# Performance work log

Measured on AMD Instinct MI355X. Metric: run time of the kernel, lower is better.

## Reference

```python
import jax, jax.numpy as jnp
import numpy as np

B, C, N, H, W = 8, 128, 16, 56, 56
HID, OUT = 128, 128


def conv1x1(x, w, b):
    # 1x1x1 Conv3d == channel-mixing GEMM. x: [B,Cin,N,H,W], w: [Cout,Cin], b: [Cout]
    return jnp.einsum('oc,bcnhw->bonhw', w, x) + b[None, :, None, None, None]


def setup_inputs() -> dict:
    key = jax.random.key(0)
    ks = jax.random.split(key, 9)
    s = 0.02
    return {
        'x': jax.random.normal(ks[0], (B, C, N, H, W), dtype=jnp.float32),
        'w_q': jax.random.normal(ks[1], (HID, C), dtype=jnp.float32) * s,
        'b_q': jax.random.normal(ks[2], (HID,), dtype=jnp.float32) * s,
        'w_k': jax.random.normal(ks[3], (HID, C), dtype=jnp.float32) * s,
        'b_k': jax.random.normal(ks[4], (HID,), dtype=jnp.float32) * s,
        'w_v': jax.random.normal(ks[5], (HID, C), dtype=jnp.float32) * s,
        'b_v': jax.random.normal(ks[6], (HID,), dtype=jnp.float32) * s,
        'w_o': jax.random.normal(ks[7], (OUT, HID), dtype=jnp.float32) * s,
        'b_o': jax.random.normal(ks[8], (OUT,), dtype=jnp.float32) * s,
    }


def reference(x, w_q, b_q, w_k, b_k, w_v, b_v, w_o, b_o):
    Bsz, Cc, Nn, Hh, Ww = x.shape
    L = Nn * Hh * Ww
    q = conv1x1(x, w_q, b_q).reshape(Bsz, -1, L)   # [B, hid, L]
    k = conv1x1(x, w_k, b_k).reshape(Bsz, -1, L)   # [B, hid, L]
    v = conv1x1(x, w_v, b_v).reshape(Bsz, -1, L)   # [B, hid, L]
    # NOTE: attention is over CHANNELS (hid x hid), since k was transposed to [B, L, hid]
    attn = jax.nn.softmax(jnp.einsum('bql,bkl->bqk', q, k), axis=-1)  # [B, hid, hid]
    feats = jnp.einsum('bqk,bkl->bql', attn, v).reshape(Bsz, -1, Nn, Hh, Ww)
    out = conv1x1(feats, w_o, b_o) + x             # residual requires out_dim == in_dim
    return jnp.mean(out, axis=2)                   # mean over N (depth) -> [B, out, H, W]
```

## Files before the change

kernel.cpp:

```cpp
#include <hip/hip_runtime.h>
#include <hip/hip_bf16.h>
#include <cstdint>

#define BB   8
#define CCH  128
#define NND  16
#define HWD  3136
#define LLT  50176
#define HWB  64
#define NHB  49

#define OFF_SP  0
#define OFF_RP  6422528
#define OFF_S   6472704
#define OFF_M   6603776
#define OFF_Q   6734848
#define OFF_AV  6865920
#define OFF_CV  6866944

typedef __attribute__((ext_vector_type(8)))  short bf16x8;
typedef __attribute__((ext_vector_type(16))) float f32x16;

__device__ __forceinline__ uint32_t fbits(float f){ union{float f;uint32_t u;}v; v.f=f; return v.u; }
__device__ __forceinline__ float bitsf(uint32_t u){ union{uint32_t u;float f;}v; v.u=u; return v.f; }

#define MFMA32(a,b,c) __builtin_amdgcn_mfma_f32_32x32x16_bf16((a),(b),(c),0,0,0)

__global__ __launch_bounds__(256,2) void k1_gram(const float* __restrict__ x,
    float* __restrict__ Sp, float* __restrict__ rp, float* __restrict__ Y)
{
  __shared__ __align__(16) short lds_h[2][8*128*8];
  __shared__ __align__(16) short lds_l[2][8*128*8];
  const int b   = blockIdx.x / NHB;
  const int hb  = blockIdx.x % NHB;
  const int hw0 = hb * HWB;
  const int tid = threadIdx.x;
  const int lane = tid & 63, w = tid >> 6;
  const int wr = w >> 1, wc = w & 1;
  const int rr  = tid >> 1, h = tid & 1;
  const float* xb = x + (size_t)b*CCH*LLT + (size_t)rr*LLT + hw0 + 32*h;

  f32x16 acc[2][2];
  #pragma unroll
  for(int ai=0;ai<2;ai++)
    #pragma unroll
    for(int bi=0;bi<2;bi++)
      #pragma unroll
      for(int e=0;e<16;e++) acc[ai][bi][e] = 0.f;
  float yac[32];
  #pragma unroll
  for(int i=0;i<32;i++) yac[i]=0.f;

  float4 v[8];
  #pragma unroll
  for(int u=0;u<8;u++) v[u] = *(const float4*)(xb + 4*u);

#define SPLIT(bufi)                                                         \
  {                                                                         \
    _Pragma("unroll")                                                       \
    for(int c2=0;c2<4;c2++){                                                \
      int hwd_[4], lwd_[4];                                                 \
      _Pragma("unroll")                                                     \
      for(int q=0;q<2;q++){                                                 \
        const int u = 2*c2+q;                                               \
        const float x0=v[u].x, x1=v[u].y, x2=v[u].z, x3=v[u].w;             \
        const uint32_t a0=fbits(x0),a1=fbits(x1),a2=fbits(x2),a3=fbits(x3); \
        hwd_[2*q+0] = __builtin_amdgcn_perm(a1, a0, 0x07060302u);           \
        hwd_[2*q+1] = __builtin_amdgcn_perm(a3, a2, 0x07060302u);           \
        const float l0 = x0 - bitsf(a0&0xFFFF0000u);                        \
        const float l1 = x1 - bitsf(a1&0xFFFF0000u);                        \
        const float l2 = x2 - bitsf(a2&0xFFFF0000u);                        \
        const float l3 = x3 - bitsf(a3&0xFFFF0000u);                        \
        lwd_[2*q+0] = __builtin_amdgcn_perm(fbits(l1), fbits(l0), 0x07060302u); \
        lwd_[2*q+1] = __builtin_amdgcn_perm(fbits(l3), fbits(l2), 0x07060302u); \
        yac[4*u+0]+=x0; yac[4*u+1]+=x1; yac[4*u+2]+=x2; yac[4*u+3]+=x3;     \
      }                                                                     \
      const int kc = 4*h + c2;                                              \
      *(int4*)&lds_h[bufi][(kc*128 + rr)*8] = make_int4(hwd_[0],hwd_[1],hwd_[2],hwd_[3]); \
      *(int4*)&lds_l[bufi][(kc*128 + rr)*8] = make_int4(lwd_[0],lwd_[1],lwd_[2],lwd_[3]); \
    }                                                                       \
  }

  SPLIT(0);
  __syncthreads();
  #pragma unroll
  for(int u=0;u<8;u++) v[u] = *(const float4*)(xb + HWD + 4*u);

  for(int n=0;n<NND;n++){
    const int cur = n & 1;
    #pragma unroll
    for(int ks=0;ks<4;ks++){
      const int kc = 2*ks + (lane>>5);
      const int rbase = (kc*128 + (lane&31))*8;
      const bf16x8 a0h = *(const bf16x8*)&lds_h[cur][rbase + (64*wr    )*8];
      const bf16x8 a0l = *(const bf16x8*)&lds_l[cur][rbase + (64*wr    )*8];
      const bf16x8 a1h = *(const bf16x8*)&lds_h[cur][rbase + (64*wr+32)*8];
      const bf16x8 a1l = *(const bf16x8*)&lds_l[cur][rbase + (64*wr+32)*8];
      const bf16x8 b0h = *(const bf16x8*)&lds_h[cur][rbase + (64*wc    )*8];
      const bf16x8 b0l = *(const bf16x8*)&lds_l[cur][rbase + (64*wc    )*8];
      const bf16x8 b1h = *(const bf16x8*)&lds_h[cur][rbase + (64*wc+32)*8];
      const bf16x8 b1l = *(const bf16x8*)&lds_l[cur][rbase + (64*wc+32)*8];
      acc[0][0] = MFMA32(a0h, b0h, acc[0][0]);
      acc[0][0] = MFMA32(a0h, b0l, acc[0][0]);
      acc[0][0] = MFMA32(a0l, b0h, acc[0][0]);
      acc[0][1] = MFMA32(a0h, b1h, acc[0][1]);
      acc[0][1] = MFMA32(a0h, b1l, acc[0][1]);
      acc[0][1] = MFMA32(a0l, b1h, acc[0][1]);
      acc[1][0] = MFMA32(a1h, b0h, acc[1][0]);
      acc[1][0] = MFMA32(a1h, b0l, acc[1][0]);
      acc[1][0] = MFMA32(a1l, b0h, acc[1][0]);
      acc[1][1] = MFMA32(a1h, b1h, acc[1][1]);
      acc[1][1] = MFMA32(a1h, b1l, acc[1][1]);
      acc[1][1] = MFMA32(a1l, b1h, acc[1][1]);
    }
    if(n+1 < NND){
      SPLIT(cur^1);
      __syncthreads();
      if(n+2 < NND){
        #pragma unroll
        for(int u=0;u<8;u++) v[u] = *(const float4*)(xb + (size_t)(n+2)*HWD + 4*u);
      }
    }
  }
#undef SPLIT

  #pragma unroll
  for(int u=0;u<8;u++){
    float4 o4 = make_float4(yac[4*u]*0.0625f, yac[4*u+1]*0.0625f,
                            yac[4*u+2]*0.0625f, yac[4*u+3]*0.0625f);
    *(float4*)(Y + ((size_t)b*CCH + rr)*HWD + hw0 + 32*h + 4*u) = o4;
  }
  float p = 0.f;
  #pragma unroll
  for(int i=0;i<32;i++) p += yac[i];
  p += __shfl_xor(p, 1);
  if(h==0) rp[(size_t)(b*NHB+hb)*CCH + rr] = p;

  float* Sb = Sp + (size_t)(b*NHB+hb)*CCH*CCH;
  const int col = lane & 31, roff = 4*(lane>>5);
  #pragma unroll
  for(int ai=0;ai<2;ai++)
    #pragma unroll
    for(int bi=0;bi<2;bi++)
      #pragma unroll
      for(int reg=0;reg<16;reg++){
        const int row = 64*wr + 32*ai + roff + (reg&3) + 8*(reg>>2);
        Sb[(size_t)row*CCH + 64*wc + 32*bi + col] = acc[ai][bi][reg];
      }
}

__global__ __launch_bounds__(256) void k1r(const float* __restrict__ Sp,
                                           float* __restrict__ S)
{
  const int b  = blockIdx.x >> 4;
  const int ch = blockIdx.x & 15;
  const int i  = ch*1024 + threadIdx.x*4;
  const float* p = Sp + (size_t)b*NHB*CCH*CCH + i;
  float4 s = make_float4(0.f,0.f,0.f,0.f);
  for(int hb=0;hb<NHB;hb++){
    float4 v = *(const float4*)(p + (size_t)hb*CCH*CCH);
    s.x+=v.x; s.y+=v.y; s.z+=v.z; s.w+=v.w;
  }
  *(float4*)(S + (size_t)b*CCH*CCH + i) = s;
}

__global__ __launch_bounds__(256) void k2ab(const float* __restrict__ S, const float* __restrict__ rp,
    const float* __restrict__ wq, const float* __restrict__ bq,
    const float* __restrict__ wk, const float* __restrict__ bk,
    const float* __restrict__ wv, const float* __restrict__ bv,
    float* __restrict__ M, float* __restrict__ av)
{
  __shared__ __align__(16) float t1[16][132];
  __shared__ float rb_s[CCH];
  __shared__ float wrk_s[CCH];
  __shared__ float wrq_s[16];
  const int b   = blockIdx.x >> 3;
  const int r0  = (blockIdx.x & 7) * 16;
  const int tid = threadIdx.x;
  const float* Sb = S + (size_t)b*CCH*CCH;

  if(tid < CCH){
    float s = 0.f;
    const float* rpb = rp + (size_t)b*NHB*CCH + tid;
    for(int hb=0;hb<NHB;hb++) s += rpb[hb*CCH];
    rb_s[tid] = s;
  }
  __syncthreads();

  if(tid < CCH){
    float s = 0.f;
    for(int m=0;m<CCH;m++) s += wk[(size_t)tid*CCH+m]*rb_s[m];
    wrk_s[tid] = s;
  } else if(tid < CCH+16){
    const int rr2 = tid - CCH;
    float s = 0.f;
    for(int m=0;m<CCH;m++) s += wq[(size_t)(r0+rr2)*CCH+m]*rb_s[m];
    wrq_s[rr2] = s;
  }

  const int rr = tid >> 4;
  const int c0 = (tid & 15) * 8;
  {
    float a8[8] = {0,0,0,0,0,0,0,0};
    const float* wqr = wq + (size_t)(r0+rr)*CCH;
    for(int m4=0;m4<32;m4++){
      float4 w4 = *(const float4*)(wqr + 4*m4);
      const float wl[4] = {w4.x,w4.y,w4.z,w4.w};
      #pragma unroll
      for(int mm=0;mm<4;mm++){
        const int m = 4*m4+mm;
        const float w = wl[mm];
        float4 s0 = *(const float4*)(Sb + (size_t)m*CCH + c0);
        float4 s1 = *(const float4*)(Sb + (size_t)m*CCH + c0 + 4);
        a8[0]=fmaf(w,s0.x,a8[0]); a8[1]=fmaf(w,s0.y,a8[1]);
        a8[2]=fmaf(w,s0.z,a8[2]); a8[3]=fmaf(w,s0.w,a8[3]);
        a8[4]=fmaf(w,s1.x,a8[4]); a8[5]=fmaf(w,s1.y,a8[5]);
        a8[6]=fmaf(w,s1.z,a8[6]); a8[7]=fmaf(w,s1.w,a8[7]);
      }
    }
    #pragma unroll
    for(int j=0;j<8;j++) t1[rr][c0+j] = a8[j];
  }
  __syncthreads();

  const int j0 = c0;
  float g[8] = {0,0,0,0,0,0,0,0};
  for(int c4=0;c4<32;c4++){
    float4 tv = *(const float4*)(&t1[rr][4*c4]);
    #pragma unroll
    for(int jj=0;jj<8;jj++){
      float4 w4 = *(const float4*)(wk + (size_t)(j0+jj)*CCH + 4*c4);
      g[jj]=fmaf(tv.x,w4.x,g[jj]); g[jj]=fmaf(tv.y,w4.y,g[jj]);
      g[jj]=fmaf(tv.z,w4.z,g[jj]); g[jj]=fmaf(tv.w,w4.w,g[jj]);
    }
  }
  const float bqr  = bq[r0+rr];
  const float wrqr = wrq_s[rr];
  #pragma unroll
  for(int jj=0;jj<8;jj++)
    g[jj] += wrqr*bk[j0+jj] + bqr*wrk_s[j0+jj] + (float)LLT*bqr*bk[j0+jj];

  float mx = g[0];
  #pragma unroll
  for(int jj=1;jj<8;jj++) mx = fmaxf(mx, g[jj]);
  #pragma unroll
  for(int s=1;s<16;s<<=1) mx = fmaxf(mx, __shfl_xor(mx, s, 16));
  float ex[8], sum=0.f;
  #pragma unroll
  for(int jj=0;jj<8;jj++){ ex[jj] = expf(g[jj]-mx); sum += ex[jj]; }
  #pragma unroll
  for(int s=1;s<16;s<<=1) sum += __shfl_xor(sum, s, 16);
  const float inv = 1.0f/sum;

  float pa = 0.f;
  #pragma unroll
  for(int jj=0;jj<8;jj++) pa += ex[jj]*inv*bv[j0+jj];
  #pragma unroll
  for(int s=1;s<16;s<<=1) pa += __shfl_xor(pa, s, 16);
  if((tid&15)==0) av[b*CCH + r0+rr] = pa;

  __syncthreads();
  #pragma unroll
  for(int jj=0;jj<8;jj++) t1[rr][j0+jj] = ex[jj]*inv;
  __syncthreads();

  {
    float a8[8] = {0,0,0,0,0,0,0,0};
    for(int k4=0;k4<32;k4++){
      float4 a4 = *(const float4*)(&t1[rr][4*k4]);
      const float al[4] = {a4.x,a4.y,a4.z,a4.w};
      #pragma unroll
      for(int kk=0;kk<4;kk++){
        const int k = 4*k4+kk;
        const float wgt = al[kk];
        float4 v0 = *(const float4*)(wv + (size_t)k*CCH + c0);
        float4 v1 = *(const float4*)(wv + (size_t)k*CCH + c0 + 4);
        a8[0]=fmaf(wgt,v0.x,a8[0]); a8[1]=fmaf(wgt,v0.y,a8[1]);
        a8[2]=fmaf(wgt,v0.z,a8[2]); a8[3]=fmaf(wgt,v0.w,a8[3]);
        a8[4]=fmaf(wgt,v1.x,a8[4]); a8[5]=fmaf(wgt,v1.y,a8[5]);
        a8[6]=fmaf(wgt,v1.z,a8[6]); a8[7]=fmaf(wgt,v1.w,a8[7]);
      }
    }
    float* Mr = M + ((size_t)b*CCH + r0+rr)*CCH + c0;
    *(float4*)(Mr  ) = make_float4(a8[0],a8[1],a8[2],a8[3]);
    *(float4*)(Mr+4) = make_float4(a8[4],a8[5],a8[6],a8[7]);
  }
}

__global__ __launch_bounds__(256) void k2c(const float* __restrict__ M,
    const float* __restrict__ wo, const float* __restrict__ bo,
    const float* __restrict__ av, float* __restrict__ Q, float* __restrict__ cv)
{
  const int b  = blockIdx.x >> 3;
  const int o0 = (blockIdx.x & 7)*16;
  const int tid = threadIdx.x;
  const int rr = tid>>4, c0 = (tid&15)*8;
  const int o  = o0 + rr;
  const float* wor = wo + (size_t)o*CCH;
  const float* Mb  = M + (size_t)b*CCH*CCH;
  float a8[8] = {0,0,0,0,0,0,0,0};
  for(int m4=0;m4<32;m4++){
    float4 w4 = *(const float4*)(wor + 4*m4);
    const float wl[4] = {w4.x,w4.y,w4.z,w4.w};
    #pragma unroll
    for(int mm=0;mm<4;mm++){
      const int m = 4*m4+mm;
      const float w = wl[mm];
      float4 v0 = *(const float4*)(Mb + (size_t)m*CCH + c0);
      float4 v1 = *(const float4*)(Mb + (size_t)m*CCH + c0 + 4);
      a8[0]=fmaf(w,v0.x,a8[0]); a8[1]=fmaf(w,v0.y,a8[1]);
      a8[2]=fmaf(w,v0.z,a8[2]); a8[3]=fmaf(w,v0.w,a8[3]);
      a8[4]=fmaf(w,v1.x,a8[4]); a8[5]=fmaf(w,v1.y,a8[5]);
      a8[6]=fmaf(w,v1.z,a8[6]); a8[7]=fmaf(w,v1.w,a8[7]);
    }
  }
  #pragma unroll
  for(int j=0;j<8;j++) if(o == c0+j) a8[j] += 1.0f;
  float* Qr = Q + ((size_t)b*CCH + o)*CCH + c0;
  *(float4*)(Qr  ) = make_float4(a8[0],a8[1],a8[2],a8[3]);
  *(float4*)(Qr+4) = make_float4(a8[4],a8[5],a8[6],a8[7]);

  if(tid < 16){
    const int oo = o0 + tid;
    float s = 0.f;
    for(int m=0;m<CCH;m++) s += wo[(size_t)oo*CCH+m]*av[b*CCH+m];
    cv[b*CCH + oo] = s + bo[oo];
  }
}

__global__ __launch_bounds__(256,2) void k3(const float* __restrict__ Q,
    const float* __restrict__ cv, float* __restrict__ out)
{
  __shared__ __align__(16) float4 qs[4096];
  const int b   = blockIdx.x / NHB;
  const int hb  = blockIdx.x % NHB;
  const int hw0 = hb * HWB;
  const int tid = threadIdx.x;

  const float4* Qg = (const float4*)(Q + (size_t)b*CCH*CCH);
  #pragma unroll
  for(int it=0; it<16; it++){
    const int idx = it*256 + tid;
    const int row = idx >> 5, ch = idx & 31;
    qs[(row<<5) | (ch ^ (row>>3))] = Qg[idx];
  }
  __syncthreads();

  const int tx = tid & 15, ty = tid >> 4;
  const int o0 = tx*8;
  const int hg = ty*4;
  float acc[8][4];
  #pragma unroll
  for(int i=0;i<8;i++){ acc[i][0]=0.f; acc[i][1]=0.f; acc[i][2]=0.f; acc[i][3]=0.f; }

  const float* Yb = out + (size_t)b*CCH*HWD + hw0 + hg;
  for(int c4=0;c4<32;c4++){
    float4 yv[4];
    #pragma unroll
    for(int mm=0;mm<4;mm++) yv[mm] = *(const float4*)(Yb + (size_t)(4*c4+mm)*HWD);
    #pragma unroll
    for(int i=0;i<8;i++){
      const int row = o0 + i;
      const float4 q4 = qs[(row<<5) | (c4 ^ tx)];
      const float ql[4] = {q4.x,q4.y,q4.z,q4.w};
      #pragma unroll
      for(int mm=0;mm<4;mm++){
        acc[i][0]=fmaf(ql[mm],yv[mm].x,acc[i][0]);
        acc[i][1]=fmaf(ql[mm],yv[mm].y,acc[i][1]);
        acc[i][2]=fmaf(ql[mm],yv[mm].z,acc[i][2]);
        acc[i][3]=fmaf(ql[mm],yv[mm].w,acc[i][3]);
      }
    }
  }
  __syncthreads();
  #pragma unroll
  for(int i=0;i<8;i++){
    const float c = cv[b*CCH + o0+i];
    float4 o4 = make_float4(acc[i][0]+c, acc[i][1]+c, acc[i][2]+c, acc[i][3]+c);
    *(float4*)(out + ((size_t)b*CCH + o0+i)*HWD + hw0 + hg) = o4;
  }
}

extern "C" void kernel_launch(void* const* d_in, const int* in_sizes, int n_in,
                              void* d_out, int out_size, void* d_ws, size_t ws_size,
                              hipStream_t stream) {
  const float* x  = (const float*)d_in[0];
  const float* wq = (const float*)d_in[1];
  const float* bq = (const float*)d_in[2];
  const float* wk = (const float*)d_in[3];
  const float* bk = (const float*)d_in[4];
  const float* wv = (const float*)d_in[5];
  const float* bv = (const float*)d_in[6];
  const float* wo = (const float*)d_in[7];
  const float* bo = (const float*)d_in[8];
  float* out = (float*)d_out;
  float* ws  = (float*)d_ws;

  k1_gram<<<BB*NHB, 256, 0, stream>>>(x, ws+OFF_SP, ws+OFF_RP, out);
  k1r<<<128, 256, 0, stream>>>(ws+OFF_SP, ws+OFF_S);
  k2ab<<<64, 256, 0, stream>>>(ws+OFF_S, ws+OFF_RP, wq, bq, wk, bk, wv, bv,
                               ws+OFF_M, ws+OFF_AV);
  k2c<<<64, 256, 0, stream>>>(ws+OFF_M, wo, bo, ws+OFF_AV, ws+OFF_Q, ws+OFF_CV);
  k3<<<BB*NHB, 256, 0, stream>>>(ws+OFF_Q, ws+OFF_CV, out);
}
```

Before: 145.9 us.

## Exploit Gram matrix symmetry: compute only lower-triangle tiles and mirror in reduction

The Gram kernel now computes only the 10 lower-triangular 32x32 tiles of the symmetric 128x128 channel Gram matrix instead of all 16, split unevenly across the four waves. This cuts MFMA work by roughly 40% and shrinks the partial-sum workspace and reduction traffic. The reduction kernel sums per-tile partials and writes each off-diagonal tile plus its transpose via LDS. The cost is load imbalance across waves (three tiles for two waves, two for the others) and a divergent branch on wave id.

```diff
diff --git a/kernel.cpp b/kernel.cpp
--- a/kernel.cpp
+++ b/kernel.cpp
@@ -9,14 +9,16 @@
 #define LLT  50176
 #define HWB  64
 #define NHB  49
+#define K3WB 64
+#define K3NB 49
 
 #define OFF_SP  0
-#define OFF_RP  6422528
-#define OFF_S   6472704
-#define OFF_M   6603776
-#define OFF_Q   6734848
-#define OFF_AV  6865920
-#define OFF_CV  6866944
+#define OFF_S   4014080
+#define OFF_RP  4145152
+#define OFF_M   4195328
+#define OFF_Q   4326400
+#define OFF_AV  4457472
+#define OFF_CV  4458496
 
 typedef __attribute__((ext_vector_type(8)))  short bf16x8;
 typedef __attribute__((ext_vector_type(16))) float f32x16;
@@ -36,17 +38,12 @@
   const int hw0 = hb * HWB;
   const int tid = threadIdx.x;
   const int lane = tid & 63, w = tid >> 6;
-  const int wr = w >> 1, wc = w & 1;
   const int rr  = tid >> 1, h = tid & 1;
   const float* xb = x + (size_t)b*CCH*LLT + (size_t)rr*LLT + hw0 + 32*h;
 
-  f32x16 acc[2][2];
-  #pragma unroll
-  for(int ai=0;ai<2;ai++)
-    #pragma unroll
-    for(int bi=0;bi<2;bi++)
-      #pragma unroll
-      for(int e=0;e<16;e++) acc[ai][bi][e] = 0.f;
+  f32x16 a0, a1, a2;
+  #pragma unroll
+  for(int e=0;e<16;e++){ a0[e]=0.f; a1[e]=0.f; a2[e]=0.f; }
   float yac[32];
   #pragma unroll
   for(int i=0;i<32;i++) yac[i]=0.f;
@@ -64,13 +61,13 @@
       for(int q=0;q<2;q++){                                                 \
         const int u = 2*c2+q;                                               \
         const float x0=v[u].x, x1=v[u].y, x2=v[u].z, x3=v[u].w;             \
-        const uint32_t a0=fbits(x0),a1=fbits(x1),a2=fbits(x2),a3=fbits(x3); \
-        hwd_[2*q+0] = __builtin_amdgcn_perm(a1, a0, 0x07060302u);           \
-        hwd_[2*q+1] = __builtin_amdgcn_perm(a3, a2, 0x07060302u);           \
-        const float l0 = x0 - bitsf(a0&0xFFFF0000u);                        \
-        const float l1 = x1 - bitsf(a1&0xFFFF0000u);                        \
-        const float l2 = x2 - bitsf(a2&0xFFFF0000u);                        \
-        const float l3 = x3 - bitsf(a3&0xFFFF0000u);                        \
+        const uint32_t b0=fbits(x0),b1=fbits(x1),b2=fbits(x2),b3=fbits(x3); \
+        hwd_[2*q+0] = __builtin_amdgcn_perm(b1, b0, 0x07060302u);           \
+        hwd_[2*q+1] = __builtin_amdgcn_perm(b3, b2, 0x07060302u);           \
+        const float l0 = x0 - bitsf(b0&0xFFFF0000u);                        \
+        const float l1 = x1 - bitsf(b1&0xFFFF0000u);                        \
+        const float l2 = x2 - bitsf(b2&0xFFFF0000u);                        \
+        const float l3 = x3 - bitsf(b3&0xFFFF0000u);                        \
         lwd_[2*q+0] = __builtin_amdgcn_perm(fbits(l1), fbits(l0), 0x07060302u); \
         lwd_[2*q+1] = __builtin_amdgcn_perm(fbits(l3), fbits(l2), 0x07060302u); \
         yac[4*u+0]+=x0; yac[4*u+1]+=x1; yac[4*u+2]+=x2; yac[4*u+3]+=x3;     \
@@ -81,6 +78,15 @@
     }                                                                       \
   }
 
+#define FR(g)                                                               \
+  const bf16x8 f##g##h = *(const bf16x8*)&lds_h[cur][(kcb + 32*g)*8];       \
+  const bf16x8 f##g##l = *(const bf16x8*)&lds_l[cur][(kcb + 32*g)*8];
+
+#define TILE(A, gi, gj)                                                     \
+  A = MFMA32(f##gi##h, f##gj##h, A);                                        \
+  A = MFMA32(f##gi##h, f##gj##l, A);                                        \
+  A = MFMA32(f##gi##l, f##gj##h, A);
+
   SPLIT(0);
   __syncthreads();
   #pragma unroll
@@ -90,28 +96,20 @@
     const int cur = n & 1;
     #pragma unroll
     for(int ks=0;ks<4;ks++){
-      const int kc = 2*ks + (lane>>5);
-      const int rbase = (kc*128 + (lane&31))*8;
-      const bf16x8 a0h = *(const bf16x8*)&lds_h[cur][rbase + (64*wr    )*8];
-      const bf16x8 a0l = *(const bf16x8*)&lds_l[cur][rbase + (64*wr    )*8];
-      const bf16x8 a1h = *(const bf16x8*)&lds_h[cur][rbase + (64*wr+32)*8];
-      const bf16x8 a1l = *(const bf16x8*)&lds_l[cur][rbase + (64*wr+32)*8];
-      const bf16x8 b0h = *(const bf16x8*)&lds_h[cur][rbase + (64*wc    )*8];
-      const bf16x8 b0l = *(const bf16x8*)&lds_l[cur][rbase + (64*wc    )*8];
-      const bf16x8 b1h = *(const bf16x8*)&lds_h[cur][rbase + (64*wc+32)*8];
-      const bf16x8 b1l = *(const bf16x8*)&lds_l[cur][rbase + (64*wc+32)*8];
-      acc[0][0] = MFMA32(a0h, b0h, acc[0][0]);
-      acc[0][0] = MFMA32(a0h, b0l, acc[0][0]);
-      acc[0][0] = MFMA32(a0l, b0h, acc[0][0]);
-      acc[0][1] = MFMA32(a0h, b1h, acc[0][1]);
-      acc[0][1] = MFMA32(a0h, b1l, acc[0][1]);
-      acc[0][1] = MFMA32(a0l, b1h, acc[0][1]);
-      acc[1][0] = MFMA32(a1h, b0h, acc[1][0]);
-      acc[1][0] = MFMA32(a1h, b0l, acc[1][0]);
-      acc[1][0] = MFMA32(a1l, b0h, acc[1][0]);
-      acc[1][1] = MFMA32(a1h, b1h, acc[1][1]);
-      acc[1][1] = MFMA32(a1h, b1l, acc[1][1]);
-      acc[1][1] = MFMA32(a1l, b1h, acc[1][1]);
+      const int kcb = (2*ks + (lane>>5))*128 + (lane&31);
+      if(w==0){
+        FR(0) FR(1)
+        TILE(a0,0,0) TILE(a1,1,0) TILE(a2,1,1)
+      } else if(w==1){
+        FR(0) FR(1) FR(2)
+        TILE(a0,2,0) TILE(a1,2,1) TILE(a2,2,2)
+      } else if(w==2){
+        FR(0) FR(1) FR(3)
+        TILE(a0,3,0) TILE(a1,3,1)
+      } else {
+        FR(2) FR(3)
+        TILE(a0,3,2) TILE(a1,3,3)
+      }
     }
     if(n+1 < NND){
       SPLIT(cur^1);
@@ -123,6 +121,8 @@
     }
   }
 #undef SPLIT
+#undef FR
+#undef TILE
 
   #pragma unroll
   for(int u=0;u<8;u++){
@@ -136,32 +136,49 @@
   p += __shfl_xor(p, 1);
   if(h==0) rp[(size_t)(b*NHB+hb)*CCH + rr] = p;
 
-  float* Sb = Sp + (size_t)(b*NHB+hb)*CCH*CCH;
+  const int slot0 = (w<2) ? 3*w : 2*w+2;
+  float* Sb = Sp + ((size_t)blockIdx.x*10 + slot0)*1024;
   const int col = lane & 31, roff = 4*(lane>>5);
-  #pragma unroll
-  for(int ai=0;ai<2;ai++)
-    #pragma unroll
-    for(int bi=0;bi<2;bi++)
-      #pragma unroll
-      for(int reg=0;reg<16;reg++){
-        const int row = 64*wr + 32*ai + roff + (reg&3) + 8*(reg>>2);
-        Sb[(size_t)row*CCH + 64*wc + 32*bi + col] = acc[ai][bi][reg];
-      }
-}
-
-__global__ __launch_bounds__(256) void k1r(const float* __restrict__ Sp,
-                                           float* __restrict__ S)
+#define STORE(A, s)                                                         \
+  { _Pragma("unroll")                                                       \
+    for(int reg=0;reg<16;reg++){                                            \
+      const int row = roff + (reg&3) + 8*(reg>>2);                          \
+      Sb[(s)*1024 + row*32 + col] = A[reg];                                 \
+    } }
+  STORE(a0, 0)
+  STORE(a1, 1)
+  if(w<2) STORE(a2, 2)
+#undef STORE
+}
+
+__global__ __launch_bounds__(256) void k1rs(const float* __restrict__ Sp,
+                                            float* __restrict__ S)
 {
-  const int b  = blockIdx.x >> 4;
-  const int ch = blockIdx.x & 15;
-  const int i  = ch*1024 + threadIdx.x*4;
-  const float* p = Sp + (size_t)b*NHB*CCH*CCH + i;
+  __shared__ float tl[32*33];
+  const int b = blockIdx.x/10, t = blockIdx.x%10;
+  const int tid = threadIdx.x;
+  int i, j;
+  if(t<1){ i=0; j=t; } else if(t<3){ i=1; j=t-1; }
+  else if(t<6){ i=2; j=t-3; } else { i=3; j=t-6; }
+
   float4 s = make_float4(0.f,0.f,0.f,0.f);
-  for(int hb=0;hb<NHB;hb++){
-    float4 v = *(const float4*)(p + (size_t)hb*CCH*CCH);
+  const float* p = Sp + ((size_t)(b*NHB)*10 + t)*1024 + 4*tid;
+  for(int wdw=0; wdw<NHB; wdw++){
+    float4 v = *(const float4*)(p + (size_t)wdw*10240);
     s.x+=v.x; s.y+=v.y; s.z+=v.z; s.w+=v.w;
   }
-  *(float4*)(S + (size_t)b*CCH*CCH + i) = s;
+  const int r = (4*tid) >> 5, c = (4*tid) & 31;
+  *(float4*)&S[(size_t)b*CCH*CCH + (size_t)(32*i+r)*CCH + 32*j + c] = s;
+  if(i != j){
+    tl[r*33 + c+0] = s.x; tl[r*33 + c+1] = s.y;
+    tl[r*33 + c+2] = s.z; tl[r*33 + c+3] = s.w;
+    __syncthreads();
+    const int r2 = tid>>3, c2 = 4*(tid&7);
+    float4 o;
+    o.x = tl[(c2+0)*33 + r2]; o.y = tl[(c2+1)*33 + r2];
+    o.z = tl[(c2+2)*33 + r2]; o.w = tl[(c2+3)*33 + r2];
+    *(float4*)&S[(size_t)b*CCH*CCH + (size_t)(32*j+r2)*CCH + 32*i + c2] = o;
+  }
 }
 
 __global__ __launch_bounds__(256) void k2ab(const float* __restrict__ S, const float* __restrict__ rp,
@@ -332,9 +349,9 @@
     const float* __restrict__ cv, float* __restrict__ out)
 {
   __shared__ __align__(16) float4 qs[4096];
-  const int b   = blockIdx.x / NHB;
-  const int hb  = blockIdx.x % NHB;
-  const int hw0 = hb * HWB;
+  const int b   = blockIdx.x / K3NB;
+  const int hb  = blockIdx.x % K3NB;
+  const int hw0 = hb * K3WB;
   const int tid = threadIdx.x;
 
   const float4* Qg = (const float4*)(Q + (size_t)b*CCH*CCH);
@@ -397,9 +414,9 @@
   float* ws  = (float*)d_ws;
 
   k1_gram<<<BB*NHB, 256, 0, stream>>>(x, ws+OFF_SP, ws+OFF_RP, out);
-  k1r<<<128, 256, 0, stream>>>(ws+OFF_SP, ws+OFF_S);
-  k2ab<<<64, 256, 0, stream>>>(ws+OFF_S, ws+OFF_RP, wq, bq, wk, bk, wv, bv,
-                               ws+OFF_M, ws+OFF_AV);
-  k2c<<<64, 256, 0, stream>>>(ws+OFF_M, wo, bo, ws+OFF_AV, ws+OFF_Q, ws+OFF_CV);
-  k3<<<BB*NHB, 256, 0, stream>>>(ws+OFF_Q, ws+OFF_CV, out);
-}
+  k1rs  <<<80, 256, 0, stream>>>(ws+OFF_SP, ws+OFF_S);
+  k2ab  <<<64, 256, 0, stream>>>(ws+OFF_S, ws+OFF_RP, wq, bq, wk, bk, wv, bv,
+                                 ws+OFF_M, ws+OFF_AV);
+  k2c   <<<64, 256, 0, stream>>>(ws+OFF_M, wo, bo, ws+OFF_AV, ws+OFF_Q, ws+OFF_CV);
+  k3    <<<BB*K3NB, 256, 0, stream>>>(ws+OFF_Q, ws+OFF_CV, out);
+}
```

After: 149.3 us. 1.02x slower.
